# Kernel tuning notes

Hardware: AMD Instinct MI355X
Metric: run time of the kernel (lower is better)

The kernel has to match this reference:

```python
import jax, jax.numpy as jnp
import numpy as np

N_NODES = 50000


def _norm_adj(num_nodes, edge_index):
    # Append self loops, compute symmetric normalization values per edge.
    row, col = edge_index[0], edge_index[1]
    loop = jnp.arange(num_nodes, dtype=edge_index.dtype)
    row = jnp.concatenate([row, loop])
    col = jnp.concatenate([col, loop])
    ones = jnp.ones(row.shape[0], dtype=jnp.float32)
    deg = jax.ops.segment_sum(ones, row, num_segments=num_nodes)  # row-sum of A (duplicates summed, as coalesce does)
    dinv = jnp.clip(deg, 1.0) ** -0.5
    v = dinv[row] * dinv[col]  # [E + N]
    return row, col, v


def _spmm(row, col, v, x, num_nodes):
    # y[i] = sum_{e: row[e]=i} v[e] * x[col[e]]  (duplicate edges sum, matching coalesced sparse mm)
    return jax.ops.segment_sum(v[:, None] * x[col], row, num_segments=num_nodes)


def setup_inputs() -> dict:
    key = jax.random.key(0)
    ks = jax.random.split(key, 6)
    in_dim, hidden_dim, out_dim = 128, 256, 128
    n_edges = 800000
    x = jax.random.normal(ks[0], (N_NODES, in_dim), dtype=jnp.float32)
    edge_index = jax.random.randint(ks[1], (2, n_edges), 0, N_NODES, dtype=jnp.int32)
    W1 = jax.random.normal(ks[2], (hidden_dim, in_dim), dtype=jnp.float32) * (1.0 / np.sqrt(in_dim))
    b1 = jax.random.normal(ks[3], (hidden_dim,), dtype=jnp.float32) * 0.01
    W2 = jax.random.normal(ks[4], (out_dim, hidden_dim), dtype=jnp.float32) * (1.0 / np.sqrt(hidden_dim))
    b2 = jax.random.normal(ks[5], (out_dim,), dtype=jnp.float32) * 0.01
    return {"x": x, "edge_index": edge_index, "W1": W1, "b1": b1, "W2": W2, "b2": b2}


def reference(x, edge_index, W1, b1, W2, b2):
    n = x.shape[0]
    row, col, v = _norm_adj(n, edge_index)
    h = _spmm(row, col, v, x, n)            # A @ x
    h = jax.nn.relu(h @ W1.T + b1)           # lin1 + relu (dropout is eval no-op)
    h = _spmm(row, col, v, h, n)             # A @ h
    return h @ W2.T + b2                     # lin2
```

## Files before the change

kernel.cpp:

```cpp
#include <hip/hip_runtime.h>
#include <hip/hip_bf16.h>

#define NNODES 50000
#define DIM 128
#define NBUCK 196
#define BCAP 8192

typedef unsigned short u16;
typedef _Float16 f16;
typedef float  f32x4  __attribute__((ext_vector_type(4)));
typedef _Float16 f16x4v __attribute__((ext_vector_type(4)));
typedef _Float16 f16x8 __attribute__((ext_vector_type(8)));

#define MFMAH(a, b, c) __builtin_amdgcn_mfma_f32_16x16x32_f16((a), (b), (c), 0, 0, 0)

__global__ __launch_bounds__(256) void init_misc(int* __restrict__ gcursor,
        const float* __restrict__ W1, const float* __restrict__ W2,
        f16* __restrict__ w1h, f16* __restrict__ w2h,
        f16* __restrict__ xs, f16* __restrict__ zs, int n) {
    int b = blockIdx.x, t = threadIdx.x;
    if (b == 0) {
        gcursor[t] = t * BCAP;
    } else if (b <= 32) {
        int i = (b - 1) * 256 + t;
        float4 v = reinterpret_cast<const float4*>(W1)[i];
        f16x4v o = { (f16)v.x, (f16)v.y, (f16)v.z, (f16)v.w };
        reinterpret_cast<f16x4v*>(w1h)[i] = o;
    } else if (b <= 64) {
        int i = (b - 33) * 256 + t;
        float4 v = reinterpret_cast<const float4*>(W2)[i];
        f16x4v o = { (f16)v.x, (f16)v.y, (f16)v.z, (f16)v.w };
        reinterpret_cast<f16x4v*>(w2h)[i] = o;
    } else {
        f16x4v o = {};
        if (t < 32)      reinterpret_cast<f16x4v*>(xs)[(size_t)n * 32 + t] = o;
        else if (t < 64) reinterpret_cast<f16x4v*>(zs)[(size_t)n * 32 + (t - 32)] = o;
    }
}

__global__ __launch_bounds__(256) void bucket_place(const int* __restrict__ row,
                                                    const int* __restrict__ col,
                                                    int* __restrict__ gcursor,
                                                    unsigned* __restrict__ bkt, int nE) {
    __shared__ int hist[256];
    __shared__ int cur[256];
    int t = threadIdx.x;
    hist[t] = 0;
    __syncthreads();
    unsigned pk[8]; int valid = 0;
    int base_e = blockIdx.x * 2048 + t;
    #pragma unroll
    for (int k = 0; k < 8; ++k) {
        int e = base_e + k * 256;
        if (e < nE) {
            unsigned r = (unsigned)row[e], c = (unsigned)col[e];
            pk[k] = (r << 16) | c;
            valid |= 1 << k;
            atomicAdd(&hist[r >> 8], 1);
        }
    }
    __syncthreads();
    if (hist[t] > 0) cur[t] = atomicAdd(&gcursor[t], hist[t]);
    __syncthreads();
    #pragma unroll
    for (int k = 0; k < 8; ++k) {
        if (valid & (1 << k)) {
            int pos = atomicAdd(&cur[pk[k] >> 24], 1);
            bkt[pos] = pk[k];
        }
    }
}

__global__ __launch_bounds__(256) void csr_fill(const unsigned* __restrict__ bkt,
                                                const int* __restrict__ gcursor,
                                                const float* __restrict__ x,
                                                int2* __restrict__ row_rng,
                                                float* __restrict__ dinv,
                                                u16* __restrict__ cols16,
                                                f16* __restrict__ xs, int n) {
    __shared__ int lcnt[256], lscan[256], lcur[256];
    __shared__ float ldinv[256];
    int b = blockIdx.x, t = threadIdx.x;
    int r0 = b << 8;
    int s = b * BCAP, e = gcursor[b];
    lcnt[t] = 0;
    __syncthreads();
    for (int i = s + t; i < e; i += 256)
        atomicAdd(&lcnt[(bkt[i] >> 16) & 255], 1);
    __syncthreads();
    int v = lcnt[t];
    lscan[t] = v;
    __syncthreads();
    for (int off = 1; off < 256; off <<= 1) {
        int u = (t >= off) ? lscan[t - off] : 0;
        __syncthreads();
        lscan[t] += u;
        __syncthreads();
    }
    int gpos = s + lscan[t] - v;
    int r = r0 + t;
    float dval = rsqrtf((float)(v + 1));
    if (r < n) {
        row_rng[r] = make_int2(gpos, gpos + v);
        dinv[r] = dval;
    }
    ldinv[t] = dval;
    lcur[t] = gpos;
    __syncthreads();
    for (int i = s + t; i < e; i += 256) {
        unsigned rc = bkt[i];
        int pos = atomicAdd(&lcur[(rc >> 16) & 255], 1);
        cols16[pos] = (u16)(rc & 0xffffu);
    }
    int nrows = min(256, n - r0);
    int totq = nrows * 32;
    for (int q = t; q < totq; q += 256) {
        int rl = q >> 5;
        float d = ldinv[rl];
        float4 vx = reinterpret_cast<const float4*>(x)[(size_t)(r0 + rl) * 32 + (q & 31)];
        f16x4v o = { (f16)(d * vx.x), (f16)(d * vx.y), (f16)(d * vx.z), (f16)(d * vx.w) };
        reinterpret_cast<f16x4v*>(xs)[(size_t)(r0 + rl) * 32 + (q & 31)] = o;
    }
}

template <bool OUT16, bool BIAS>
__global__ __launch_bounds__(256) void spmm_gather(const int2* __restrict__ row_rng,
                         const u16* __restrict__ cols16,
                         const f16* __restrict__ Xs, const float* __restrict__ dinv,
                         const float* __restrict__ bias,
                         float* __restrict__ Y, f16* __restrict__ Yh, int n) {
    int tid = blockIdx.x * blockDim.x + threadIdx.x;
    int i = tid >> 5;
    int l = tid & 31;
    if (i >= n) return;
    const f16x4v* X4 = reinterpret_cast<const f16x4v*>(Xs);
    int2 rng = row_rng[i];
    float di = dinv[i];
    f16x4v xv = X4[(size_t)i * 32 + l];
    float4 acc;
    acc.x = (float)xv[0]; acc.y = (float)xv[1];
    acc.z = (float)xv[2]; acc.w = (float)xv[3];
    int s = rng.x, e = rng.y;
    for (int j = s; j < e; j += 16) {
        int c[16];
        #pragma unroll
        for (int t = 0; t < 16; ++t) {
            int idx = j + t;
            bool ok = idx < e;
            int cc = (int)cols16[ok ? idx : (e - 1)];
            c[t] = ok ? cc : n;
        }
        f16x4v g[16];
        #pragma unroll
        for (int t = 0; t < 16; ++t) g[t] = X4[(size_t)c[t] * 32 + l];
        #pragma unroll
        for (int t = 0; t < 16; ++t) {
            acc.x += (float)g[t][0];
            acc.y += (float)g[t][1];
            acc.z += (float)g[t][2];
            acc.w += (float)g[t][3];
        }
    }
    acc.x *= di; acc.y *= di; acc.z *= di; acc.w *= di;
    if (BIAS) {
        float4 b = reinterpret_cast<const float4*>(bias)[l];
        acc.x += b.x; acc.y += b.y; acc.z += b.z; acc.w += b.w;
    }
    if (OUT16) {
        f16x4v o = { (f16)acc.x, (f16)acc.y, (f16)acc.z, (f16)acc.w };
        *reinterpret_cast<f16x4v*>(&Yh[(size_t)i * DIM + l * 4]) = o;
    } else {
        reinterpret_cast<float4*>(Y)[(size_t)i * 32 + l] = acc;
    }
}

__global__ __launch_bounds__(256, 2) void mlp_fused(
        const f16* __restrict__ y1, const f16* __restrict__ w1,
        const float* __restrict__ b1, const f16* __restrict__ w2,
        const float* __restrict__ dinv, f16* __restrict__ zs, int M) {
    constexpr int HSTR = 264;
    __shared__ f16 hl[4][32][HSTR];
    const int wave = threadIdx.x >> 6;
    const int lane = threadIdx.x & 63;
    const int lr = lane & 15;
    const int lq = lane >> 4;
    const int mbase = blockIdx.x * 128 + wave * 32;

    f16x8 yb[2][4];
    #pragma unroll
    for (int nf = 0; nf < 2; ++nf) {
        int r = min(mbase + nf * 16 + lr, M - 1);
        const f16* pr = y1 + (size_t)r * 128 + lq * 8;
        #pragma unroll
        for (int ks = 0; ks < 4; ++ks)
            yb[nf][ks] = *reinterpret_cast<const f16x8*>(pr + ks * 32);
    }

    #pragma unroll 1
    for (int q = 0; q < 4; ++q) {
        const int hc0 = q * 64;
        f16x8 wa[4][4];
        #pragma unroll
        for (int mf = 0; mf < 4; ++mf) {
            const f16* pw = w1 + (size_t)(hc0 + mf * 16 + lr) * 128 + lq * 8;
            #pragma unroll
            for (int ks = 0; ks < 4; ++ks)
                wa[mf][ks] = *reinterpret_cast<const f16x8*>(pw + ks * 32);
        }
        f32x4 acc[4][2] = {};
        #pragma unroll
        for (int ks = 0; ks < 4; ++ks)
            #pragma unroll
            for (int mf = 0; mf < 4; ++mf)
                #pragma unroll
                for (int nf = 0; nf < 2; ++nf)
                    acc[mf][nf] = MFMAH(wa[mf][ks], yb[nf][ks], acc[mf][nf]);
        #pragma unroll
        for (int mf = 0; mf < 4; ++mf) {
            float4 bb = *reinterpret_cast<const float4*>(&b1[hc0 + mf * 16 + lq * 4]);
            #pragma unroll
            for (int nf = 0; nf < 2; ++nf) {
                f16x4v hv = { (f16)fmaxf(acc[mf][nf][0] + bb.x, 0.f),
                              (f16)fmaxf(acc[mf][nf][1] + bb.y, 0.f),
                              (f16)fmaxf(acc[mf][nf][2] + bb.z, 0.f),
                              (f16)fmaxf(acc[mf][nf][3] + bb.w, 0.f) };
                *reinterpret_cast<f16x4v*>(&hl[wave][nf * 16 + lr][hc0 + mf * 16 + lq * 4]) = hv;
            }
        }
    }

    f32x4 acc2[8][2] = {};
    #pragma unroll 1
    for (int ks = 0; ks < 8; ++ks) {
        f16x8 hb[2];
        #pragma unroll
        for (int nf = 0; nf < 2; ++nf)
            hb[nf] = *reinterpret_cast<const f16x8*>(&hl[wave][nf * 16 + lr][ks * 32 + lq * 8]);
        f16x8 wa2[8];
        #pragma unroll
        for (int mf = 0; mf < 8; ++mf)
            wa2[mf] = *reinterpret_cast<const f16x8*>(w2 + (size_t)(mf * 16 + lr) * 256 + ks * 32 + lq * 8);
        #pragma unroll
        for (int mf = 0; mf < 8; ++mf)
            #pragma unroll
            for (int nf = 0; nf < 2; ++nf)
                acc2[mf][nf] = MFMAH(wa2[mf], hb[nf], acc2[mf][nf]);
    }
    #pragma unroll
    for (int nf = 0; nf < 2; ++nf) {
        int node = mbase + nf * 16 + lr;
        if (node >= M) continue;
        float dn = dinv[node];
        #pragma unroll
        for (int mf = 0; mf < 8; ++mf) {
            f16x4v zv = { (f16)(dn * acc2[mf][nf][0]), (f16)(dn * acc2[mf][nf][1]),
                          (f16)(dn * acc2[mf][nf][2]), (f16)(dn * acc2[mf][nf][3]) };
            *reinterpret_cast<f16x4v*>(zs + (size_t)node * 128 + mf * 16 + lq * 4) = zv;
        }
    }
}

extern "C" void kernel_launch(void* const* d_in, const int* in_sizes, int n_in,
                              void* d_out, int out_size, void* d_ws, size_t ws_size,
                              hipStream_t stream) {
    const float* x  = (const float*)d_in[0];
    const int*   ei = (const int*)d_in[1];
    const float* W1 = (const float*)d_in[2];
    const float* b1 = (const float*)d_in[3];
    const float* W2 = (const float*)d_in[4];
    const float* b2 = (const float*)d_in[5];
    float* out = (float*)d_out;

    const int N = NNODES;
    const int E = in_sizes[1] / 2;
    const int IN_D = 128, HID = 256;
    const int* row = ei;
    const int* col = ei + E;

    char* ws = (char*)d_ws;
    size_t off = 0;
    auto carve = [&](size_t bytes) { void* p = ws + off; off += (bytes + 255) & ~size_t(255); return p; };
    int*      gcursor = (int*)carve((size_t)256 * 4);
    int2*     row_rng = (int2*)carve((size_t)N * 8);
    float*    dinv    = (float*)carve((size_t)N * 4);
    unsigned* bkt     = (unsigned*)carve((size_t)NBUCK * BCAP * 4);
    u16*      cols16  = (u16*)carve((size_t)NBUCK * BCAP * 2);
    f16*      w1h     = (f16*)carve((size_t)HID * IN_D * 2);
    f16*      w2h     = (f16*)carve((size_t)IN_D * HID * 2);
    f16*      xs      = (f16*)carve((size_t)(N + 1) * IN_D * 2);
    f16*      y1h     = (f16*)carve((size_t)(N + 1) * IN_D * 2);
    f16*      zsh     = y1h;

    const int TB = 256;
    const int eblk = (E + 2047) / 2048;

    init_misc<<<66, TB, 0, stream>>>(gcursor, W1, W2, w1h, w2h, xs, zsh, N);
    bucket_place<<<eblk, TB, 0, stream>>>(row, col, gcursor, bkt, E);
    csr_fill<<<NBUCK, TB, 0, stream>>>(bkt, gcursor, x, row_rng, dinv, cols16, xs, N);

    spmm_gather<true, false><<<(N * 32 + TB - 1) / TB, TB, 0, stream>>>(
        row_rng, cols16, xs, dinv, nullptr, nullptr, y1h, N);

    mlp_fused<<<(N + 127) / 128, 256, 0, stream>>>(y1h, w1h, b1, w2h, dinv, zsh, N);

    spmm_gather<false, true><<<(N * 32 + TB - 1) / TB, TB, 0, stream>>>(
        row_rng, cols16, zsh, dinv, b2, out, nullptr, N);
}
```

Measured before the change: 145.5 us.

## Sort CSR columns by coarse column bin and remap SpMM blocks per XCD

The CSR fill kernel now sub-bins each row's edges into 8 coarse column ranges, so the column list within a row is roughly ordered by source node. The gather kernel remaps block IDs so that consecutive row blocks land on the same XCD. Together these aim to improve L2 locality of the random feature gathers across the chiplets. The cost is extra shared-memory atomics and a small per-row scan in the CSR build.

```diff
diff --git a/kernel.cpp b/kernel.cpp
--- a/kernel.cpp
+++ b/kernel.cpp
@@ -78,17 +78,25 @@
                                                 float* __restrict__ dinv,
                                                 u16* __restrict__ cols16,
                                                 f16* __restrict__ xs, int n) {
-    __shared__ int lcnt[256], lscan[256], lcur[256];
+    __shared__ int lrow[256], lscan[256];
+    __shared__ int lbin[256][8];
     __shared__ float ldinv[256];
     int b = blockIdx.x, t = threadIdx.x;
     int r0 = b << 8;
     int s = b * BCAP, e = gcursor[b];
-    lcnt[t] = 0;
-    __syncthreads();
-    for (int i = s + t; i < e; i += 256)
-        atomicAdd(&lcnt[(bkt[i] >> 16) & 255], 1);
-    __syncthreads();
-    int v = lcnt[t];
+    lrow[t] = 0;
+    #pragma unroll
+    for (int k = 0; k < 8; ++k) lbin[t][k] = 0;
+    __syncthreads();
+    for (int i = s + t; i < e; i += 256) {
+        unsigned rc = bkt[i];
+        int rl = (rc >> 16) & 255;
+        int ch = (rc & 0xffffu) >> 13;
+        atomicAdd(&lrow[rl], 1);
+        atomicAdd(&lbin[rl][ch], 1);
+    }
+    __syncthreads();
+    int v = lrow[t];
     lscan[t] = v;
     __syncthreads();
     for (int off = 1; off < 256; off <<= 1) {
@@ -100,26 +108,32 @@
     int gpos = s + lscan[t] - v;
     int r = r0 + t;
     float dval = rsqrtf((float)(v + 1));
+    ldinv[t] = dval;
     if (r < n) {
         row_rng[r] = make_int2(gpos, gpos + v);
         dinv[r] = dval;
     }
-    ldinv[t] = dval;
-    lcur[t] = gpos;
+    int run = gpos;
+    #pragma unroll
+    for (int k = 0; k < 8; ++k) { int c = lbin[t][k]; lbin[t][k] = run; run += c; }
     __syncthreads();
     for (int i = s + t; i < e; i += 256) {
         unsigned rc = bkt[i];
-        int pos = atomicAdd(&lcur[(rc >> 16) & 255], 1);
+        int rl = (rc >> 16) & 255;
+        int ch = (rc & 0xffffu) >> 13;
+        int pos = atomicAdd(&lbin[rl][ch], 1);
         cols16[pos] = (u16)(rc & 0xffffu);
     }
     int nrows = min(256, n - r0);
-    int totq = nrows * 32;
-    for (int q = t; q < totq; q += 256) {
-        int rl = q >> 5;
-        float d = ldinv[rl];
-        float4 vx = reinterpret_cast<const float4*>(x)[(size_t)(r0 + rl) * 32 + (q & 31)];
-        f16x4v o = { (f16)(d * vx.x), (f16)(d * vx.y), (f16)(d * vx.z), (f16)(d * vx.w) };
-        reinterpret_cast<f16x4v*>(xs)[(size_t)(r0 + rl) * 32 + (q & 31)] = o;
+    if (nrows > 0) {
+        int totq = nrows * 32;
+        for (int q = t; q < totq; q += 256) {
+            int rl = q >> 5;
+            float d = ldinv[rl];
+            float4 vx = reinterpret_cast<const float4*>(x)[(size_t)(r0 + rl) * 32 + (q & 31)];
+            f16x4v o = { (f16)(d * vx.x), (f16)(d * vx.y), (f16)(d * vx.z), (f16)(d * vx.w) };
+            reinterpret_cast<f16x4v*>(xs)[(size_t)(r0 + rl) * 32 + (q & 31)] = o;
+        }
     }
 }
 
@@ -129,7 +143,11 @@
                          const f16* __restrict__ Xs, const float* __restrict__ dinv,
                          const float* __restrict__ bias,
                          float* __restrict__ Y, f16* __restrict__ Yh, int n) {
-    int tid = blockIdx.x * blockDim.x + threadIdx.x;
+    int nwg = gridDim.x;
+    int q = nwg >> 3, rr = nwg & 7;
+    int xcd = blockIdx.x & 7, idx = blockIdx.x >> 3;
+    int bid = (xcd < rr ? xcd * (q + 1) : rr * (q + 1) + (xcd - rr) * q) + idx;
+    int tid = bid * 256 + threadIdx.x;
     int i = tid >> 5;
     int l = tid & 31;
     if (i >= n) return;
@@ -145,9 +163,9 @@
         int c[16];
         #pragma unroll
         for (int t = 0; t < 16; ++t) {
-            int idx = j + t;
-            bool ok = idx < e;
-            int cc = (int)cols16[ok ? idx : (e - 1)];
+            int idx2 = j + t;
+            bool ok = idx2 < e;
+            int cc = (int)cols16[ok ? idx2 : (e - 1)];
             c[t] = ok ? cc : n;
         }
         f16x4v g[16];
```

After: 145.9 us. No clear change (+0.2%).

## Split feature matrices into four column slabs and gather slab-by-slab

Applied to the files above, without the earlier changes.

Stores the fp16 node feature tables as four contiguous 32-column slabs instead of row-major 128-wide rows. The SpMM gather now assigns 8 lanes per node and loops over the four slabs in sequence, so each pass only touches a quarter-width table, which may fit better in cache during random gathers. The cost is reading the column indices four times per row and having fewer concurrent gathers per node. The producer (csr_fill) and consumer (mlp_fused) are updated to match the slab layout.

```diff
diff --git a/kernel.cpp b/kernel.cpp
--- a/kernel.cpp
+++ b/kernel.cpp
@@ -5,6 +5,7 @@
 #define DIM 128
 #define NBUCK 196
 #define BCAP 8192
+#define NPASS 4
 
 typedef unsigned short u16;
 typedef _Float16 f16;
@@ -19,6 +20,7 @@
         f16* __restrict__ w1h, f16* __restrict__ w2h,
         f16* __restrict__ xs, f16* __restrict__ zs, int n) {
     int b = blockIdx.x, t = threadIdx.x;
+    size_t seg = (size_t)(n + 1) * 32;
     if (b == 0) {
         gcursor[t] = t * BCAP;
     } else if (b <= 32) {
@@ -33,8 +35,14 @@
         reinterpret_cast<f16x4v*>(w2h)[i] = o;
     } else {
         f16x4v o = {};
-        if (t < 32)      reinterpret_cast<f16x4v*>(xs)[(size_t)n * 32 + t] = o;
-        else if (t < 64) reinterpret_cast<f16x4v*>(zs)[(size_t)n * 32 + (t - 32)] = o;
+        if (t < 32) {
+            int p = t >> 3, l = t & 7;
+            reinterpret_cast<f16x4v*>(xs + (size_t)p * seg)[(size_t)n * 8 + l] = o;
+        } else if (t < 64) {
+            int tt = t - 32;
+            int p = tt >> 3, l = tt & 7;
+            reinterpret_cast<f16x4v*>(zs + (size_t)p * seg)[(size_t)n * 8 + l] = o;
+        }
     }
 }
 
@@ -83,6 +91,7 @@
     int b = blockIdx.x, t = threadIdx.x;
     int r0 = b << 8;
     int s = b * BCAP, e = gcursor[b];
+    size_t seg = (size_t)(n + 1) * 32;
     lcnt[t] = 0;
     __syncthreads();
     for (int i = s + t; i < e; i += 256)
@@ -100,11 +109,11 @@
     int gpos = s + lscan[t] - v;
     int r = r0 + t;
     float dval = rsqrtf((float)(v + 1));
+    ldinv[t] = dval;
     if (r < n) {
         row_rng[r] = make_int2(gpos, gpos + v);
         dinv[r] = dval;
     }
-    ldinv[t] = dval;
     lcur[t] = gpos;
     __syncthreads();
     for (int i = s + t; i < e; i += 256) {
@@ -113,64 +122,72 @@
         cols16[pos] = (u16)(rc & 0xffffu);
     }
     int nrows = min(256, n - r0);
-    int totq = nrows * 32;
-    for (int q = t; q < totq; q += 256) {
-        int rl = q >> 5;
-        float d = ldinv[rl];
-        float4 vx = reinterpret_cast<const float4*>(x)[(size_t)(r0 + rl) * 32 + (q & 31)];
-        f16x4v o = { (f16)(d * vx.x), (f16)(d * vx.y), (f16)(d * vx.z), (f16)(d * vx.w) };
-        reinterpret_cast<f16x4v*>(xs)[(size_t)(r0 + rl) * 32 + (q & 31)] = o;
+    if (nrows > 0) {
+        int totq = nrows * 32;
+        for (int q = t; q < totq; q += 256) {
+            int rl = q >> 5;
+            int qq = q & 31;
+            int p = qq >> 3, l = qq & 7;
+            float d = ldinv[rl];
+            float4 vx = reinterpret_cast<const float4*>(x)[(size_t)(r0 + rl) * 32 + qq];
+            f16x4v o = { (f16)(d * vx.x), (f16)(d * vx.y), (f16)(d * vx.z), (f16)(d * vx.w) };
+            reinterpret_cast<f16x4v*>(xs + (size_t)p * seg)[(size_t)(r0 + rl) * 8 + l] = o;
+        }
     }
 }
 
 template <bool OUT16, bool BIAS>
-__global__ __launch_bounds__(256) void spmm_gather(const int2* __restrict__ row_rng,
+__global__ __launch_bounds__(256, 8) void spmm_pass(const int2* __restrict__ row_rng,
                          const u16* __restrict__ cols16,
-                         const f16* __restrict__ Xs, const float* __restrict__ dinv,
+                         const f16* __restrict__ Xb, const float* __restrict__ dinv,
                          const float* __restrict__ bias,
-                         float* __restrict__ Y, f16* __restrict__ Yh, int n) {
-    int tid = blockIdx.x * blockDim.x + threadIdx.x;
-    int i = tid >> 5;
-    int l = tid & 31;
+                         float* __restrict__ Y, f16* __restrict__ Yb, int n) {
+    int tid = blockIdx.x * 256 + threadIdx.x;
+    int i = tid >> 3;
+    int l = tid & 7;
     if (i >= n) return;
-    const f16x4v* X4 = reinterpret_cast<const f16x4v*>(Xs);
     int2 rng = row_rng[i];
     float di = dinv[i];
-    f16x4v xv = X4[(size_t)i * 32 + l];
-    float4 acc;
-    acc.x = (float)xv[0]; acc.y = (float)xv[1];
-    acc.z = (float)xv[2]; acc.w = (float)xv[3];
-    int s = rng.x, e = rng.y;
-    for (int j = s; j < e; j += 16) {
-        int c[16];
-        #pragma unroll
-        for (int t = 0; t < 16; ++t) {
-            int idx = j + t;
-            bool ok = idx < e;
-            int cc = (int)cols16[ok ? idx : (e - 1)];
-            c[t] = ok ? cc : n;
-        }
-        f16x4v g[16];
-        #pragma unroll
-        for (int t = 0; t < 16; ++t) g[t] = X4[(size_t)c[t] * 32 + l];
-        #pragma unroll
-        for (int t = 0; t < 16; ++t) {
-            acc.x += (float)g[t][0];
-            acc.y += (float)g[t][1];
-            acc.z += (float)g[t][2];
-            acc.w += (float)g[t][3];
-        }
-    }
-    acc.x *= di; acc.y *= di; acc.z *= di; acc.w *= di;
-    if (BIAS) {
-        float4 b = reinterpret_cast<const float4*>(bias)[l];
-        acc.x += b.x; acc.y += b.y; acc.z += b.z; acc.w += b.w;
-    }
-    if (OUT16) {
-        f16x4v o = { (f16)acc.x, (f16)acc.y, (f16)acc.z, (f16)acc.w };
-        *reinterpret_cast<f16x4v*>(&Yh[(size_t)i * DIM + l * 4]) = o;
-    } else {
-        reinterpret_cast<float4*>(Y)[(size_t)i * 32 + l] = acc;
+    size_t seg = (size_t)(n + 1) * 32;
+    #pragma unroll 1
+    for (int p = 0; p < NPASS; ++p) {
+        const f16x4v* X4 = reinterpret_cast<const f16x4v*>(Xb + (size_t)p * seg);
+        f16x4v xv = X4[(size_t)i * 8 + l];
+        float4 acc;
+        acc.x = (float)xv[0]; acc.y = (float)xv[1];
+        acc.z = (float)xv[2]; acc.w = (float)xv[3];
+        int s = rng.x, e = rng.y;
+        for (int j = s; j < e; j += 8) {
+            int c[8];
+            #pragma unroll
+            for (int t = 0; t < 8; ++t) {
+                int idx = j + t;
+                bool ok = idx < e;
+                int cc = (int)cols16[ok ? idx : (e - 1)];
+                c[t] = ok ? cc : n;
+            }
+            f16x4v g[8];
+            #pragma unroll
+            for (int t = 0; t < 8; ++t) g[t] = X4[(size_t)c[t] * 8 + l];
+            #pragma unroll
+            for (int t = 0; t < 8; ++t) {
+                acc.x += (float)g[t][0];
+                acc.y += (float)g[t][1];
+                acc.z += (float)g[t][2];
+                acc.w += (float)g[t][3];
+            }
+        }
+        acc.x *= di; acc.y *= di; acc.z *= di; acc.w *= di;
+        if (BIAS) {
+            float4 bb = reinterpret_cast<const float4*>(bias)[p * 8 + l];
+            acc.x += bb.x; acc.y += bb.y; acc.z += bb.z; acc.w += bb.w;
+        }
+        if (OUT16) {
+            f16x4v o = { (f16)acc.x, (f16)acc.y, (f16)acc.z, (f16)acc.w };
+            reinterpret_cast<f16x4v*>(Yb + (size_t)p * seg)[(size_t)i * 8 + l] = o;
+        } else {
+            reinterpret_cast<float4*>(Y)[(size_t)i * 32 + p * 8 + l] = acc;
+        }
     }
 }
 
@@ -185,15 +202,15 @@
     const int lr = lane & 15;
     const int lq = lane >> 4;
     const int mbase = blockIdx.x * 128 + wave * 32;
+    const size_t seg = (size_t)(M + 1) * 32;
 
     f16x8 yb[2][4];
     #pragma unroll
     for (int nf = 0; nf < 2; ++nf) {
         int r = min(mbase + nf * 16 + lr, M - 1);
-        const f16* pr = y1 + (size_t)r * 128 + lq * 8;
         #pragma unroll
         for (int ks = 0; ks < 4; ++ks)
-            yb[nf][ks] = *reinterpret_cast<const f16x8*>(pr + ks * 32);
+            yb[nf][ks] = *reinterpret_cast<const f16x8*>(y1 + (size_t)ks * seg + (size_t)r * 32 + lq * 8);
     }
 
     #pragma unroll 1
@@ -253,9 +270,11 @@
         float dn = dinv[node];
         #pragma unroll
         for (int mf = 0; mf < 8; ++mf) {
+            int p = mf >> 1;
+            int qd = (mf & 1) * 4 + lq;
             f16x4v zv = { (f16)(dn * acc2[mf][nf][0]), (f16)(dn * acc2[mf][nf][1]),
                           (f16)(dn * acc2[mf][nf][2]), (f16)(dn * acc2[mf][nf][3]) };
-            *reinterpret_cast<f16x4v*>(zs + (size_t)node * 128 + mf * 16 + lq * 4) = zv;
+            reinterpret_cast<f16x4v*>(zs + (size_t)p * seg)[(size_t)node * 8 + qd] = zv;
         }
     }
 }
@@ -287,8 +306,8 @@
     u16*      cols16  = (u16*)carve((size_t)NBUCK * BCAP * 2);
     f16*      w1h     = (f16*)carve((size_t)HID * IN_D * 2);
     f16*      w2h     = (f16*)carve((size_t)IN_D * HID * 2);
-    f16*      xs      = (f16*)carve((size_t)(N + 1) * IN_D * 2);
-    f16*      y1h     = (f16*)carve((size_t)(N + 1) * IN_D * 2);
+    f16*      xs      = (f16*)carve((size_t)NPASS * (N + 1) * 32 * 2);
+    f16*      y1h     = (f16*)carve((size_t)NPASS * (N + 1) * 32 * 2);
     f16*      zsh     = y1h;
 
     const int TB = 256;
@@ -298,11 +317,11 @@
     bucket_place<<<eblk, TB, 0, stream>>>(row, col, gcursor, bkt, E);
     csr_fill<<<NBUCK, TB, 0, stream>>>(bkt, gcursor, x, row_rng, dinv, cols16, xs, N);
 
-    spmm_gather<true, false><<<(N * 32 + TB - 1) / TB, TB, 0, stream>>>(
+    spmm_pass<true, false><<<(N * 8 + TB - 1) / TB, TB, 0, stream>>>(
         row_rng, cols16, xs, dinv, nullptr, nullptr, y1h, N);
 
     mlp_fused<<<(N + 127) / 128, 256, 0, stream>>>(y1h, w1h, b1, w2h, dinv, zsh, N);
 
-    spmm_gather<false, true><<<(N * 32 + TB - 1) / TB, TB, 0, stream>>>(
+    spmm_pass<false, true><<<(N * 8 + TB - 1) / TB, TB, 0, stream>>>(
         row_rng, cols16, zsh, dinv, b2, out, nullptr, N);
 }
```

Result: slower. 167.8 us (+15.3%).
